# Performance work log

Measured on AMD Instinct MI355X. Metric: run time of the kernel, lower is better.

The kernel has to match this reference:

```python
import jax, jax.numpy as jnp
import numpy as np

B, S, D, H = 2, 2048, 1024, 16
DK = D // H  # 64


def setup_inputs() -> dict:
    key = jax.random.key(0)
    ks = jax.random.split(key, 9)
    scale = 1.0 / np.sqrt(D)
    inp = {
        "q": jax.random.normal(ks[0], (B, S, D), dtype=jnp.float32),
        "k": jax.random.normal(ks[1], (B, S, D), dtype=jnp.float32),
        "v": jax.random.normal(ks[2], (B, S, D), dtype=jnp.float32),
        "Wq": jax.random.normal(ks[3], (D, D), dtype=jnp.float32) * scale,
        "bq": jax.random.normal(ks[4], (D,), dtype=jnp.float32) * scale,
        "Wk": jax.random.normal(ks[5], (D, D), dtype=jnp.float32) * scale,
        "bk": jax.random.normal(ks[6], (D,), dtype=jnp.float32) * scale,
        "Wv": jax.random.normal(ks[7], (D, D), dtype=jnp.float32) * scale,
        "bv": jax.random.normal(ks[8], (D,), dtype=jnp.float32) * scale,
        "mask": jnp.tril(jnp.ones((S, S), dtype=jnp.int32))[None, None],  # [1,1,S,S] causal
    }
    return inp


def reference(q, k, v, Wq, bq, Wk, bk, Wv, bv, mask):
    b, s, d = q.shape
    # QKV projections -> [B, H, S, DK]
    qh = (q @ Wq + bq).reshape(b, s, H, DK).transpose(0, 2, 1, 3)
    kh = (k @ Wk + bk).reshape(b, s, H, DK).transpose(0, 2, 1, 3)
    vh = (v @ Wv + bv).reshape(b, s, H, DK).transpose(0, 2, 1, 3)
    # scores [B, H, Sq, Sk]
    scores = jnp.einsum("bhqd,bhkd->bhqk", qh, kh) / jnp.sqrt(jnp.float32(DK))
    scores = jnp.where(mask == 0, jnp.float32(-1e9), scores)
    attn = jax.nn.softmax(scores, axis=-1)  # dropout is identity at inference
    out = jnp.einsum("bhqk,bhkd->bhqd", attn, vh)
    return out.transpose(0, 2, 1, 3).reshape(b, s, d)
```

## Files before the change

kernel.cpp:

```cpp
#include <hip/hip_runtime.h>
#include <hip/hip_bf16.h>

#define D_MODEL 1024
#define SEQ 2048
#define NH 16
#define DKH 64
#define MROWS 4096

typedef __attribute__((ext_vector_type(8))) short bf16x8;
typedef __attribute__((ext_vector_type(4))) float f32x4;
typedef __attribute__((ext_vector_type(4))) int int4v;

__device__ inline short f2bf(float f) {
    __hip_bfloat16 h = __float2bfloat16(f);
    return __builtin_bit_cast(short, h);
}

#define GLOAD16(gsrc, ldst)                                                     \
    __builtin_amdgcn_global_load_lds(                                           \
        (const __attribute__((address_space(1))) void*)(gsrc),                  \
        (__attribute__((address_space(3))) void*)(ldst), 16, 0, 0)

__global__ __launch_bounds__(256) void prep_kernel(
    const float* __restrict__ q, const float* __restrict__ k,
    const float* __restrict__ v,
    const float* __restrict__ Wq, const float* __restrict__ Wk,
    const float* __restrict__ Wv,
    short* __restrict__ aqkv, short* __restrict__ Wt) {
    __shared__ float tile[32][33];
    const int bx = blockIdx.x;
    if (bx < 6144) {
        const int z = bx >> 11;
        const int blk = bx & 2047;
        const float* src = (z == 0) ? q : (z == 1) ? k : v;
        short* dst = aqkv + (size_t)z * MROWS * D_MODEL;
        const size_t i = ((size_t)blk * 256 + threadIdx.x) * 8;
        float4 f0 = *(const float4*)(src + i);
        float4 f1 = *(const float4*)(src + i + 4);
        bf16x8 p;
        p[0] = f2bf(f0.x); p[1] = f2bf(f0.y); p[2] = f2bf(f0.z); p[3] = f2bf(f0.w);
        p[4] = f2bf(f1.x); p[5] = f2bf(f1.y); p[6] = f2bf(f1.z); p[7] = f2bf(f1.w);
        *(bf16x8*)(dst + i) = p;
    } else {
        int b = bx - 6144;
        const int z = b >> 10; b &= 1023;
        const float* W = (z == 0) ? Wq : (z == 1) ? Wk : Wv;
        short* dst = Wt + (size_t)z * D_MODEL * D_MODEL;
        const int n0 = (b & 31) * 32, k0 = (b >> 5) * 32;
        const int tx = threadIdx.x & 31, ty = threadIdx.x >> 5;
        for (int i = 0; i < 4; ++i)
            tile[ty + 8 * i][tx] = W[(size_t)(k0 + ty + 8 * i) * D_MODEL + n0 + tx];
        __syncthreads();
        for (int i = 0; i < 4; ++i)
            dst[(size_t)(n0 + ty + 8 * i) * D_MODEL + k0 + tx] = f2bf(tile[tx][ty + 8 * i]);
    }
}

__global__ __launch_bounds__(256) void proj_kernel(
    const short* __restrict__ aqkv, const short* __restrict__ Wt,
    const float* __restrict__ bq, const float* __restrict__ bk, const float* __restrict__ bv,
    short* __restrict__ qh, short* __restrict__ kh, short* __restrict__ vT) {
    __shared__ short sA[2][128 * 32];
    __shared__ short sB[2][128 * 32];

    const int flat = blockIdx.x;
    const int nf = (flat & 7) * 96 + (flat >> 3);
    const int z = nf >> 8;
    const int rem = nf & 255;
    const int m0 = (rem >> 3) * 128;
    const int n0 = (rem & 7) * 128;

    const short* A = aqkv + (size_t)z * MROWS * D_MODEL;
    const short* B = Wt + (size_t)z * D_MODEL * D_MODEL;
    const float* bias = (z == 0) ? bq : (z == 1) ? bk : bv;
    short* dst = (z == 0) ? qh : (z == 1) ? kh : vT;

    const int tid = threadIdx.x;
    const int lane = tid & 63;
    const int w = tid >> 6;
    const int wr = w >> 1, wc = w & 1;
    const int lg = lane >> 4, ll = lane & 15;

    const int srow = lane >> 2;
    const int scol = ((lane & 3) ^ (srow & 3)) << 3;

    const int cs = (lg * 8) ^ ((ll & 3) << 3);

    f32x4 acc[4][4] = {};

#define STAGE(buf, kt)                                                          \
    for (int c_ = 2 * w; c_ < 2 * w + 2; ++c_) {                                \
        const int row_ = c_ * 16 + srow;                                        \
        GLOAD16(A + (size_t)(m0 + row_) * D_MODEL + (kt) * 32 + scol, &sA[buf][c_ * 512]); \
        GLOAD16(B + (size_t)(n0 + row_) * D_MODEL + (kt) * 32 + scol, &sB[buf][c_ * 512]); \
    }

    STAGE(0, 0);
    __syncthreads();
    int cur = 0;

    for (int kt = 0; kt < 32; ++kt) {
        if (kt + 1 < 32) STAGE(cur ^ 1, kt + 1);

        bf16x8 af[4], bfr[4];
        for (int i = 0; i < 4; ++i)
            af[i] = *(const bf16x8*)&sA[cur][(wr * 64 + i * 16 + ll) * 32 + cs];
        for (int j = 0; j < 4; ++j)
            bfr[j] = *(const bf16x8*)&sB[cur][(wc * 64 + j * 16 + ll) * 32 + cs];
        for (int i = 0; i < 4; ++i)
            for (int j = 0; j < 4; ++j)
                acc[i][j] = __builtin_amdgcn_mfma_f32_16x16x32_bf16(af[i], bfr[j], acc[i][j], 0, 0, 0);

        __syncthreads();
        cur ^= 1;
    }
#undef STAGE

    for (int j = 0; j < 4; ++j) {
        const int n = n0 + wc * 64 + j * 16 + ll;
        const float bn = bias[n];
        const int h = n >> 6, dk = n & 63;
        for (int i = 0; i < 4; ++i) {
            for (int rr = 0; rr < 4; ++rr) {
                const int m = m0 + wr * 64 + i * 16 + lg * 4 + rr;
                float val = acc[i][j][rr] + bn;
                if (z == 0) val *= 0.125f;
                const int b = m >> 11, s = m & 2047;
                size_t idx;
                if (z < 2) idx = (((size_t)(b * NH + h)) * SEQ + s) * DKH + dk;
                else       idx = (((size_t)(b * NH + h)) * DKH + dk) * SEQ + s;
                dst[idx] = f2bf(val);
            }
        }
    }
}

__global__ __launch_bounds__(256) void attn_kernel(
    const short* __restrict__ qh, const short* __restrict__ kh,
    const short* __restrict__ vT, float* __restrict__ out) {
    __shared__ short sK[2][64 * 64];
    __shared__ short sV[2][64 * 64];
    __shared__ short sP[4][16 * 72];

    const int flat = blockIdx.x;
    const int qt = 31 - (flat >> 5);
    const int bh = flat & 31;
    const int q0 = qt * 64;
    const int tid = threadIdx.x;
    const int w = tid >> 6;
    const int lane = tid & 63;
    const int lg = lane >> 4, ll = lane & 15;
    const int b = bh >> 4, h = bh & 15;

    const short* kbase = kh + (size_t)bh * SEQ * DKH;
    const short* vbase = vT + (size_t)bh * DKH * SEQ;

    const int srow = lane >> 3;
    const int scol = ((lane & 7) ^ srow) << 3;
    const int cs0 = ((lg * 16) ^ ((ll & 7) << 4)) >> 1;
    const int cs1 = ((64 + lg * 16) ^ ((ll & 7) << 4)) >> 1;

#define ASTAGE(buf, t)                                                          \
    for (int c_ = 2 * w; c_ < 2 * w + 2; ++c_) {                                \
        const int row_ = c_ * 8 + srow;                                         \
        GLOAD16(kbase + (size_t)((t) * 64 + row_) * DKH + scol, &sK[buf][c_ * 512]); \
        GLOAD16(vbase + (size_t)row_ * SEQ + (t) * 64 + scol, &sV[buf][c_ * 512]);   \
    }

    bf16x8 qf[2];
    {
        const short* src = qh + (((size_t)bh * SEQ) + q0 + w * 16 + ll) * DKH + lg * 8;
        qf[0] = *(const bf16x8*)(src);
        qf[1] = *(const bf16x8*)(src + 32);
    }

    f32x4 acc[4] = {};
    float l_i[4] = {0.f, 0.f, 0.f, 0.f};

    const int ntiles = qt + 1;
    int cur = 0;
    ASTAGE(0, 0);
    __syncthreads();

    for (int t = 0; t < ntiles; ++t) {
        if (t + 1 < ntiles) ASTAGE(cur ^ 1, t + 1);

        f32x4 sc[4] = {};
        __builtin_amdgcn_s_setprio(1);
        for (int j = 0; j < 4; ++j) {
            const int rb = (j * 16 + ll) * 64;
            bf16x8 kf0 = *(const bf16x8*)&sK[cur][rb + cs0];
            bf16x8 kf1 = *(const bf16x8*)&sK[cur][rb + cs1];
            sc[j] = __builtin_amdgcn_mfma_f32_16x16x32_bf16(qf[0], kf0, sc[j], 0, 0, 0);
            sc[j] = __builtin_amdgcn_mfma_f32_16x16x32_bf16(qf[1], kf1, sc[j], 0, 0, 0);
        }
        __builtin_amdgcn_s_setprio(0);

        if (t == ntiles - 1) {
            const int k0 = t * 64;
            for (int j = 0; j < 4; ++j) {
                const int key = k0 + j * 16 + ll;
                for (int r = 0; r < 4; ++r) {
                    const int qrow = q0 + w * 16 + lg * 4 + r;
                    if (key > qrow) sc[j][r] = -1e30f;
                }
            }
        }

        for (int j = 0; j < 4; ++j)
            for (int r = 0; r < 4; ++r)
                sc[j][r] = __expf(sc[j][r]);
        for (int r = 0; r < 4; ++r)
            l_i[r] += (sc[0][r] + sc[1][r]) + (sc[2][r] + sc[3][r]);

        for (int j = 0; j < 4; ++j)
            for (int r = 0; r < 4; ++r)
                sP[w][(lg * 4 + r) * 72 + j * 16 + ll] = f2bf(sc[j][r]);

        bf16x8 pf0 = *(const bf16x8*)&sP[w][ll * 72 + lg * 8];
        bf16x8 pf1 = *(const bf16x8*)&sP[w][ll * 72 + lg * 8 + 32];

        __builtin_amdgcn_s_setprio(1);
        for (int j = 0; j < 4; ++j) {
            const int rb = (j * 16 + ll) * 64;
            bf16x8 vf0 = *(const bf16x8*)&sV[cur][rb + cs0];
            bf16x8 vf1 = *(const bf16x8*)&sV[cur][rb + cs1];
            acc[j] = __builtin_amdgcn_mfma_f32_16x16x32_bf16(pf0, vf0, acc[j], 0, 0, 0);
            acc[j] = __builtin_amdgcn_mfma_f32_16x16x32_bf16(pf1, vf1, acc[j], 0, 0, 0);
        }
        __builtin_amdgcn_s_setprio(0);

        __syncthreads();
        cur ^= 1;
    }

    for (int r = 0; r < 4; ++r) {
        float ts = l_i[r];
        ts += __shfl_xor(ts, 1);
        ts += __shfl_xor(ts, 2);
        ts += __shfl_xor(ts, 4);
        ts += __shfl_xor(ts, 8);
        l_i[r] = ts;
    }
    for (int j = 0; j < 4; ++j) {
        for (int r = 0; r < 4; ++r) {
            const int qrow = q0 + w * 16 + lg * 4 + r;
            out[((size_t)(b * SEQ + qrow)) * D_MODEL + h * DKH + j * 16 + ll] =
                acc[j][r] / l_i[r];
        }
    }
#undef ASTAGE
}

extern "C" void kernel_launch(void* const* d_in, const int* in_sizes, int n_in,
                              void* d_out, int out_size, void* d_ws, size_t ws_size,
                              hipStream_t stream) {
    const float* q  = (const float*)d_in[0];
    const float* k  = (const float*)d_in[1];
    const float* v  = (const float*)d_in[2];
    const float* Wq = (const float*)d_in[3];
    const float* bq = (const float*)d_in[4];
    const float* Wk = (const float*)d_in[5];
    const float* bk = (const float*)d_in[6];
    const float* Wv = (const float*)d_in[7];
    const float* bv = (const float*)d_in[8];
    float* out = (float*)d_out;

    short* aqkv = (short*)d_ws;
    short* Wt = aqkv + (size_t)3 * MROWS * D_MODEL;
    short* qh = Wt + (size_t)3 * D_MODEL * D_MODEL;
    short* kh = qh + (size_t)MROWS * D_MODEL;
    short* vT = kh + (size_t)MROWS * D_MODEL;

    hipLaunchKernelGGL(prep_kernel, dim3(9216), dim3(256), 0, stream,
                       q, k, v, Wq, Wk, Wv, aqkv, Wt);
    hipLaunchKernelGGL(proj_kernel, dim3(768), dim3(256), 0, stream,
                       aqkv, Wt, bq, bk, bv, qh, kh, vT);
    hipLaunchKernelGGL(attn_kernel, dim3(1024), dim3(256), 0, stream, qh, kh, vT, out);
}
```

Measured before the change: 216.1 us.

## Triple-buffer projection GEMM with vmcnt-gated barriers and new LDS swizzle

Turns the projection GEMM's double-buffered LDS pipeline into a three-stage ring. Tiles are prefetched two k-steps ahead, and each step waits with a partial s_waitcnt vmcnt plus one barrier instead of a full sync after compute. The LDS XOR swizzle is also changed to a different bank-conflict pattern, keyed on the row's bit pair. This raises LDS use per block, which may lower occupancy, and depends on the hand-written vmcnt counts matching the number of outstanding loads.

```diff
diff --git a/kernel.cpp b/kernel.cpp
--- a/kernel.cpp
+++ b/kernel.cpp
@@ -60,8 +60,8 @@
     const short* __restrict__ aqkv, const short* __restrict__ Wt,
     const float* __restrict__ bq, const float* __restrict__ bk, const float* __restrict__ bv,
     short* __restrict__ qh, short* __restrict__ kh, short* __restrict__ vT) {
-    __shared__ short sA[2][128 * 32];
-    __shared__ short sB[2][128 * 32];
+    __shared__ short sA[3][128 * 32];
+    __shared__ short sB[3][128 * 32];
 
     const int flat = blockIdx.x;
     const int nf = (flat & 7) * 96 + (flat >> 3);
@@ -82,9 +82,9 @@
     const int lg = lane >> 4, ll = lane & 15;
 
     const int srow = lane >> 2;
-    const int scol = ((lane & 3) ^ (srow & 3)) << 3;
-
-    const int cs = (lg * 8) ^ ((ll & 3) << 3);
+    const int scol = ((lane & 3) ^ ((lane >> 3) & 3)) << 3;
+
+    const int cs = (lg ^ ((ll >> 1) & 3)) * 8;
 
     f32x4 acc[4][4] = {};
 
@@ -95,26 +95,44 @@
         GLOAD16(B + (size_t)(n0 + row_) * D_MODEL + (kt) * 32 + scol, &sB[buf][c_ * 512]); \
     }
 
+#define COMPUTE(buf)                                                            \
+    do {                                                                        \
+        bf16x8 af[4], bfr[4];                                                   \
+        for (int i = 0; i < 4; ++i)                                             \
+            af[i] = *(const bf16x8*)&sA[buf][(wr * 64 + i * 16 + ll) * 32 + cs];\
+        for (int j = 0; j < 4; ++j)                                             \
+            bfr[j] = *(const bf16x8*)&sB[buf][(wc * 64 + j * 16 + ll) * 32 + cs];\
+        for (int i = 0; i < 4; ++i)                                             \
+            for (int j = 0; j < 4; ++j)                                         \
+                acc[i][j] = __builtin_amdgcn_mfma_f32_16x16x32_bf16(af[i], bfr[j], acc[i][j], 0, 0, 0); \
+    } while (0)
+
     STAGE(0, 0);
-    __syncthreads();
-    int cur = 0;
-
-    for (int kt = 0; kt < 32; ++kt) {
-        if (kt + 1 < 32) STAGE(cur ^ 1, kt + 1);
-
-        bf16x8 af[4], bfr[4];
-        for (int i = 0; i < 4; ++i)
-            af[i] = *(const bf16x8*)&sA[cur][(wr * 64 + i * 16 + ll) * 32 + cs];
-        for (int j = 0; j < 4; ++j)
-            bfr[j] = *(const bf16x8*)&sB[cur][(wc * 64 + j * 16 + ll) * 32 + cs];
-        for (int i = 0; i < 4; ++i)
-            for (int j = 0; j < 4; ++j)
-                acc[i][j] = __builtin_amdgcn_mfma_f32_16x16x32_bf16(af[i], bfr[j], acc[i][j], 0, 0, 0);
-
-        __syncthreads();
-        cur ^= 1;
-    }
+    STAGE(1, 1);
+    int cur = 0, sb = 2;
+    for (int kt = 0; kt < 30; ++kt) {
+        asm volatile("s_waitcnt vmcnt(4)" ::: "memory");
+        __builtin_amdgcn_sched_barrier(0);
+        __builtin_amdgcn_s_barrier();
+        __builtin_amdgcn_sched_barrier(0);
+        STAGE(sb, kt + 2);
+        COMPUTE(cur);
+        cur = (cur == 2) ? 0 : cur + 1;
+        sb = (sb == 2) ? 0 : sb + 1;
+    }
+    asm volatile("s_waitcnt vmcnt(4)" ::: "memory");
+    __builtin_amdgcn_sched_barrier(0);
+    __builtin_amdgcn_s_barrier();
+    __builtin_amdgcn_sched_barrier(0);
+    COMPUTE(cur);
+    cur = (cur == 2) ? 0 : cur + 1;
+    asm volatile("s_waitcnt vmcnt(0)" ::: "memory");
+    __builtin_amdgcn_sched_barrier(0);
+    __builtin_amdgcn_s_barrier();
+    __builtin_amdgcn_sched_barrier(0);
+    COMPUTE(cur);
 #undef STAGE
+#undef COMPUTE
 
     for (int j = 0; j < 4; ++j) {
         const int n = n0 + wc * 64 + j * 16 + ll;
```

Result: faster. 209.6 us (-3.0%).
